# Kernel optimization log

Hardware: AMD Instinct MI355X
Metric: run time of the kernel (lower is better)

Reference implementation:

```python
import jax, jax.numpy as jnp
import numpy as np
from jax import lax

D_MODEL = 192
D_STATE = 128
D_CONV = 3
EXPAND = 2
HEADDIM = 64
NGROUPS = 1
CHUNK = 256
K = 4  # scan directions
D_INNER = EXPAND * D_MODEL          # 384
D_SSM = D_INNER                     # 384
NHEADS = D_SSM // HEADDIM           # 6
HH = K * NHEADS                     # 24 heads total (dir-major)
CONV_CH = D_SSM + 2 * NGROUPS * D_STATE + NHEADS  # 646 (conv applied to x,B,C,dt channels)
D_IN_PROJ = 2 * D_INNER + 2 * NGROUPS * D_STATE + NHEADS  # 1030
BSZ, HIMG, WIMG = 4, 64, 64


def setup_inputs() -> dict:
    key = jax.random.key(0)
    ks = jax.random.split(key, 8)
    u = jax.random.normal(ks[0], (BSZ, HIMG, WIMG, D_MODEL), jnp.float32)
    W_in = jax.random.normal(ks[1], (D_MODEL, D_IN_PROJ), jnp.float32) * 0.02
    conv_w = jax.random.normal(ks[2], (CONV_CH, 1, D_CONV, D_CONV), jnp.float32) * 0.1
    conv_b = jnp.zeros((CONV_CH,), jnp.float32)
    # dt_bias init per source: inverse-softplus of dt ~ LogUniform(1e-3, 1e-1), tiled over 4 dirs
    dt = jnp.exp(jax.random.uniform(ks[3], (NHEADS,)) * (np.log(0.1) - np.log(0.001)) + np.log(0.001))
    dt = jnp.maximum(dt, 1e-4)
    inv_dt = dt + jnp.log(-jnp.expm1(-dt))
    dt_bias = jnp.tile(inv_dt[None, :], (K, 1))  # (4, nheads)
    A = jax.random.uniform(ks[4], (NHEADS,), minval=1.0, maxval=16.0)
    A_logs = jnp.tile(jnp.log(A), (K,))          # (24,)
    Ds = jnp.ones((HH,), jnp.float32)
    norm_w = jnp.ones((D_SSM,), jnp.float32)
    W_out = jax.random.normal(ks[5], (D_INNER, D_MODEL), jnp.float32) * 0.02
    return dict(u=u, W_in=W_in, conv_w=conv_w, conv_b=conv_b, dt_bias=dt_bias,
                A_logs=A_logs, Ds=Ds, norm_w=norm_w, W_out=W_out)


def _ssd(x, dt, A, Bm, Cm, chunk):
    """Chunked selective state-space scan (Mamba2 SSD).
    x: (b,L,H,P), dt: (b,L,H) (post-softplus), A: (H,) negative scalars,
    Bm/Cm: (b,L,G,N) with heads grouped G-major (H = G*hpg)."""
    b, L, H, P = x.shape
    G, N = Bm.shape[2], Bm.shape[3]
    hpg = H // G
    nc = L // chunk
    x = x.reshape(b, nc, chunk, G, hpg, P)
    dt = dt.reshape(b, nc, chunk, G, hpg)
    Bm = Bm.reshape(b, nc, chunk, G, N)
    Cm = Cm.reshape(b, nc, chunk, G, N)
    dA = dt * A.reshape(G, hpg)                 # (b,z,c,g,h), negative
    dAc = jnp.cumsum(dA, axis=2)                # within-chunk cumsum
    dAt = jnp.transpose(dAc, (0, 1, 3, 4, 2))   # (b,z,g,h,c)
    idx = jnp.arange(chunk)
    mask = idx[:, None] >= idx[None, :]         # causal within chunk
    seg = jnp.exp(jnp.where(mask, dAt[..., :, None] - dAt[..., None, :], -1e30))  # (b,z,g,h,c,s)
    CB = jnp.einsum('bzcgn,bzsgn->bzgcs', Cm, Bm)
    xdt = x * dt[..., None]                     # dt applied at source position
    y_intra = jnp.einsum('bzghcs,bzsghp->bzcghp', CB[:, :, :, None] * seg, xdt)
    decay_last = jnp.exp(dAc[:, :, -1:] - dAc)  # (b,z,c,g,h)
    states = jnp.einsum('bzcgn,bzcghp->bzghpn', Bm, xdt * decay_last[..., None])
    cd = jnp.exp(dAc[:, :, -1])                 # (b,z,g,h) whole-chunk decay

    def step(carry, inp):
        s, c = inp
        return carry * c[..., None, None] + s, carry  # emit state entering the chunk

    _, prevs = lax.scan(step, jnp.zeros_like(states[:, 0]),
                        (jnp.swapaxes(states, 0, 1), jnp.swapaxes(cd, 0, 1)))
    prev = jnp.swapaxes(prevs, 0, 1)            # (b,z,g,h,P,N)
    y_inter = jnp.einsum('bzcgn,bzghpn->bzcghp', Cm, prev) * jnp.exp(dAc)[..., None]
    return (y_intra + y_inter).reshape(b, L, H, P)


def reference(u, W_in, conv_w, conv_b, dt_bias, A_logs, Ds, norm_w, W_out):
    B, H, W, C = u.shape
    L = H * W
    zxbcdt = u @ W_in                            # (B,H,W,1030); d_mlp == 0
    z = zxbcdt[..., :D_SSM]                      # gate
    xBCdt = zxbcdt[..., D_SSM:]                  # (B,H,W,CONV_CH)
    # depthwise 3x3 conv + SiLU (NCHW)
    xb = jnp.transpose(xBCdt, (0, 3, 1, 2))
    xb = lax.conv_general_dilated(xb, conv_w, (1, 1), 'SAME',
                                  feature_group_count=CONV_CH,
                                  dimension_numbers=('NCHW', 'OIHW', 'NCHW'))
    xb = jax.nn.silu(xb + conv_b[None, :, None, None])
    # 4 scan directions: row-major, col-major, and their reverses
    d0 = xb.reshape(B, CONV_CH, L)
    d1 = jnp.transpose(xb, (0, 1, 3, 2)).reshape(B, CONV_CH, L)
    dirs = jnp.stack([d0, d1], axis=1)
    dirs = jnp.concatenate([dirs, jnp.flip(dirs, axis=-1)], axis=1)  # (B,4,CONV_CH,L)
    seq = jnp.transpose(dirs, (0, 3, 1, 2))      # (B,L,4,CONV_CH)
    xs = seq[..., :D_SSM].reshape(B, L, HH, HEADDIM)
    Bs = seq[..., D_SSM:D_SSM + D_STATE]         # (B,L,4,N), ngroups=1 -> G=4 dirs
    Cs = seq[..., D_SSM + D_STATE:D_SSM + 2 * D_STATE]
    dts = seq[..., D_SSM + 2 * D_STATE:].reshape(B, L, HH)
    dt = jax.nn.softplus(dts + dt_bias.reshape(HH))
    A = -jnp.exp(A_logs)                         # (HH,)
    y = _ssd(xs, dt, A, Bs, Cs, CHUNK) + xs * Ds[None, None, :, None]
    y = y.reshape(B, L, K, D_SSM)
    y0 = y[:, :, 0]
    y1 = y[:, :, 1]
    y2 = jnp.flip(y[:, :, 2], axis=1)
    y3 = jnp.flip(y[:, :, 3], axis=1)
    wh1 = jnp.transpose(y1.reshape(B, W, H, D_SSM), (0, 2, 1, 3)).reshape(B, L, D_SSM)
    wh3 = jnp.transpose(y3.reshape(B, W, H, D_SSM), (0, 2, 1, 3)).reshape(B, L, D_SSM)
    out = (y0 + y2 + wh1 + wh3).reshape(B, H, W, D_SSM)
    # RMSNormGated (norm_before_gate=False, group_size = d_ssm)
    g = out * jax.nn.silu(z)
    g = g * lax.rsqrt(jnp.mean(g * g, axis=-1, keepdims=True) + 1e-5) * norm_w
    return g @ W_out
```

## Files before the change

### kernel.cpp

```cpp
#include <hip/hip_runtime.h>
#include <hip/hip_fp16.h>
#include <math.h>

#define BQ 4
#define LQ 4096
#define DM 192
#define DIP 1030
#define DSSM 384
#define DST 128
#define CCH 646
#define CH640 640
#define NHD 6
#define KDIR 4
#define NCH 16
#define CLEN 256
#define UH_ELEMS (16384 * 192)
#define WT_ELEMS (1152 * 192)
#define WO_ELEMS (192 * 384)

using half8 = __attribute__((ext_vector_type(8))) _Float16;
using half4 = __attribute__((ext_vector_type(4))) _Float16;
using f32x4 = __attribute__((ext_vector_type(4))) float;

#define XWI(pp, ss) ((pp) * 72 + ((((ss) >> 3) ^ ((pp) >> 3)) << 3) + ((ss) & 7))
#define XW2(n, ss) ((n) * 72 + (((((ss) >> 3) ^ ((n) >> 3)) & 7) << 3) + ((ss) & 7))

__device__ __forceinline__ int pixof(int k, int t) {
  switch (k) {
    case 0: return t;
    case 1: return ((t & 63) << 6) | (t >> 6);
    case 2: return 4095 - t;
    default: { int tp = 4095 - t; return ((tp & 63) << 6) | (tp >> 6); }
  }
}

__device__ __forceinline__ float softplusf(float x) {
  return (x > 20.f) ? x : log1pf(expf(x));
}
__device__ __forceinline__ float siluf(float x) {
  return x / (1.f + __expf(-x));
}

__global__ void k_cvt(const float* __restrict__ u, const float* __restrict__ W,
                      const float* __restrict__ Wout,
                      _Float16* __restrict__ uh, _Float16* __restrict__ whT,
                      _Float16* __restrict__ woT) {
  int idx = blockIdx.x * 256 + threadIdx.x;
  if (idx < UH_ELEMS) uh[idx] = (_Float16)u[idx];
  int widx = idx - UH_ELEMS;
  if (widx >= 0 && widx < WT_ELEMS) {
    int n = widx / 192, kk = widx - n * 192;
    whT[widx] = (n < DIP) ? (_Float16)W[(size_t)kk * DIP + n] : (_Float16)0.f;
  }
  int wo = idx - UH_ELEMS - WT_ELEMS;
  if (wo >= 0 && wo < WO_ELEMS) {
    int n = wo / 384, kk = wo - n * 384;
    woT[wo] = (_Float16)Wout[(size_t)kk * DM + n];
  }
}

__global__ __launch_bounds__(256) void k_inproj(
    const _Float16* __restrict__ uh, const _Float16* __restrict__ whT,
    __half* __restrict__ zh, __half* __restrict__ xbch, float* __restrict__ xdt32) {
  __shared__ __align__(16) _Float16 sA[128 * 72];
  __shared__ __align__(16) _Float16 sB[128 * 72];
  int nt = blockIdx.x, mt = blockIdx.y;
  int m0 = mt * 128, n0 = nt * 128;
  int t = threadIdx.x, lane = t & 63, w = t >> 6;
  int acol = lane & 15, koff = (lane >> 4) * 8;
  int wr = w >> 1, wc = w & 1;
  f32x4 zz = {0.f, 0.f, 0.f, 0.f};
  f32x4 acc[4][4];
#pragma unroll
  for (int fr = 0; fr < 4; ++fr)
#pragma unroll
    for (int fc = 0; fc < 4; ++fc) acc[fr][fc] = zz;
  for (int kk = 0; kk < 3; ++kk) {
    if (kk) __syncthreads();
#pragma unroll
    for (int i = 0; i < 4; ++i) {
      int task = t + i * 256;
      int row = task >> 3, oct = task & 7;
      *(half8*)&sA[row * 72 + oct * 8] =
          *(const half8*)&uh[(size_t)(m0 + row) * 192 + kk * 64 + oct * 8];
      *(half8*)&sB[row * 72 + oct * 8] =
          *(const half8*)&whT[(size_t)(n0 + row) * 192 + kk * 64 + oct * 8];
    }
    __syncthreads();
#pragma unroll
    for (int ks = 0; ks < 2; ++ks) {
      half8 af[4], bf[4];
#pragma unroll
      for (int f = 0; f < 4; ++f) {
        af[f] = *(const half8*)&sA[(wr * 64 + f * 16 + acol) * 72 + ks * 32 + koff];
        bf[f] = *(const half8*)&sB[(wc * 64 + f * 16 + acol) * 72 + ks * 32 + koff];
      }
#pragma unroll
      for (int fr = 0; fr < 4; ++fr)
#pragma unroll
        for (int fc = 0; fc < 4; ++fc)
          acc[fr][fc] = __builtin_amdgcn_mfma_f32_16x16x32_f16(af[fr], bf[fc], acc[fr][fc], 0, 0, 0);
    }
  }
  int rb = (lane >> 4) * 4;
#pragma unroll
  for (int fr = 0; fr < 4; ++fr) {
#pragma unroll
    for (int fc = 0; fc < 4; ++fc) {
      int n = n0 + wc * 64 + fc * 16 + acol;
#pragma unroll
      for (int r = 0; r < 4; ++r) {
        int m = m0 + wr * 64 + fr * 16 + rb + r;
        float v = acc[fr][fc][r];
        if (n < DSSM) zh[(size_t)m * DSSM + n] = (__half)v;
        else if (n < 1024) xbch[(size_t)m * CH640 + (n - DSSM)] = (__half)v;
        else if (n < DIP) xdt32[(size_t)m * NHD + (n - 1024)] = v;
      }
    }
  }
}

__global__ void k_conv(const __half* __restrict__ xbch, const float* __restrict__ xdt,
                       const float* __restrict__ cw, const float* __restrict__ cb,
                       __half* __restrict__ convh, float* __restrict__ dtraw) {
  int pid = blockIdx.x;
  int b = pid >> 12, p = pid & 4095;
  int y = p >> 6, x = p & 63;
  int t = threadIdx.x;
  const __half2* baseh2 = (const __half2*)(xbch + (size_t)b * LQ * CH640);
  __half2* outh2 = (__half2*)(convh + (size_t)pid * CH640);
  for (int pc = t; pc < 320; pc += 256) {
    int c0 = pc * 2;
    float s0 = 0.f, s1 = 0.f;
#pragma unroll
    for (int ky = 0; ky < 3; ++ky) {
      int yy = y + ky - 1;
      if (yy < 0 || yy > 63) continue;
#pragma unroll
      for (int kx = 0; kx < 3; ++kx) {
        int xx = x + kx - 1;
        if (xx < 0 || xx > 63) continue;
        __half2 v = baseh2[(size_t)(yy * 64 + xx) * 320 + pc];
        int wi = ky * 3 + kx;
        s0 += (float)v.x * cw[c0 * 9 + wi];
        s1 += (float)v.y * cw[(c0 + 1) * 9 + wi];
      }
    }
    __half2 o;
    o.x = (__half)siluf(s0 + cb[c0]);
    o.y = (__half)siluf(s1 + cb[c0 + 1]);
    outh2[pc] = o;
  }
  if (t < NHD) {
    const float* based = xdt + (size_t)b * LQ * NHD;
    float s = 0.f;
#pragma unroll
    for (int ky = 0; ky < 3; ++ky) {
      int yy = y + ky - 1;
      if (yy < 0 || yy > 63) continue;
#pragma unroll
      for (int kx = 0; kx < 3; ++kx) {
        int xx = x + kx - 1;
        if (xx < 0 || xx > 63) continue;
        s += based[(size_t)(yy * 64 + xx) * NHD + t] * cw[(CH640 + t) * 9 + ky * 3 + kx];
      }
    }
    dtraw[(size_t)pid * NHD + t] = siluf(s + cb[CH640 + t]);
  }
}

__global__ void k_prep(const float* __restrict__ dtraw, const float* __restrict__ dt_bias,
                       const float* __restrict__ A_logs,
                       float* __restrict__ dtb, float* __restrict__ dacb) {
  __shared__ float sb[CLEN];
  int z = blockIdx.x, k = blockIdx.y, b = blockIdx.z;
  int s = threadIdx.x;
  int pixel = pixof(k, z * CLEN + s);
  const float* row = dtraw + ((size_t)(b * LQ + pixel)) * NHD;
  float raw[NHD];
#pragma unroll
  for (int h = 0; h < NHD; ++h) raw[h] = row[h];
  size_t base = (((size_t)(b * KDIR + k) * NCH + z) * NHD) * CLEN;
  for (int h = 0; h < NHD; ++h) {
    float dtv = softplusf(raw[h] + dt_bias[k * NHD + h]);
    float dA = dtv * (-expf(A_logs[k * NHD + h]));
    sb[s] = dA;
    __syncthreads();
    for (int off = 1; off < CLEN; off <<= 1) {
      float v = (s >= off) ? sb[s - off] : 0.f;
      __syncthreads();
      sb[s] += v;
      __syncthreads();
    }
    dtb[base + (size_t)h * CLEN + s] = dtv;
    dacb[base + (size_t)h * CLEN + s] = sb[s];
    __syncthreads();
  }
}

__global__ __launch_bounds__(256, 4) void k_cb(const _Float16* __restrict__ convh,
                                               _Float16* __restrict__ cbuf) {
  __shared__ __align__(16) char smem[34816];
  _Float16* sCt = (_Float16*)smem;
  _Float16* sBt = (_Float16*)(smem + 17408);
  int pi = blockIdx.x, z = blockIdx.y, bk = blockIdx.z;
  int b = bk >> 2, kd = bk & 3;
  int SI = 0;
  while ((SI + 1) * (SI + 2) / 2 <= pi) ++SI;
  int SJ = pi - SI * (SI + 1) / 2;
  int t = threadIdx.x, lane = t & 63, w = t >> 6;
  int acol = lane & 15, koff = (lane >> 4) * 8;
  int R = w * 16, arow = R + acol, rbase = R + (lane >> 4) * 4;
  const _Float16* convb = convh + (size_t)b * LQ * CH640;
  for (int i = 0; i < 4; ++i) {
    int c = t + i * 256;
    int row = c >> 4, seg = c & 15;
    int pc = pixof(kd, z * CLEN + SI * 64 + row);
    *(half8*)&sCt[row * 136 + seg * 8] =
        *(const half8*)&convb[(size_t)pc * CH640 + (DSSM + DST) + seg * 8];
    int pbx = pixof(kd, z * CLEN + SJ * 64 + row);
    *(half8*)&sBt[row * 136 + seg * 8] =
        *(const half8*)&convb[(size_t)pbx * CH640 + DSSM + seg * 8];
  }
  __syncthreads();
  f32x4 zz = {0.f, 0.f, 0.f, 0.f};
  f32x4 acc[4] = {zz, zz, zz, zz};
  for (int ks = 0; ks < 4; ++ks) {
    half8 a = *(const half8*)&sCt[arow * 136 + ks * 32 + koff];
#pragma unroll
    for (int cg = 0; cg < 4; ++cg) {
      half8 bf = *(const half8*)&sBt[(cg * 16 + acol) * 136 + ks * 32 + koff];
      acc[cg] = __builtin_amdgcn_mfma_f32_16x16x32_f16(a, bf, acc[cg], 0, 0, 0);
    }
  }
  size_t base = ((size_t)(bk * NCH + z) * 10 + pi) * 4096;
#pragma unroll
  for (int cg = 0; cg < 4; ++cg)
#pragma unroll
    for (int r = 0; r < 4; ++r)
      cbuf[base + (size_t)(rbase + r) * 64 + cg * 16 + acol] = (_Float16)acc[cg][r];
}

__global__ void k_diag(const _Float16* __restrict__ cbuf, const float* __restrict__ dacb,
                       _Float16* __restrict__ dbuf) {
  __shared__ float sd[64];
  int hs = blockIdx.x;
  int si = hs / 6, h = hs % 6;
  int z = blockIdx.y, bk = blockIdx.z;
  int t = threadIdx.x;
  if (t < 64) sd[t] = dacb[(((size_t)bk * NCH + z) * NHD + h) * CLEN + si * 64 + t];
  __syncthreads();
  size_t cb = ((size_t)(bk * NCH + z) * 10 + si * (si + 1) / 2 + si) * 4096;
  size_t db = (((size_t)(bk * NCH + z) * 4 + si) * NHD + h) * 4096;
#pragma unroll
  for (int i = 0; i < 16; ++i) {
    int e = t + i * 256;
    int sl = e >> 6, ss = e & 63;
    _Float16 v = (_Float16)0.f;
    if (ss <= sl) v = (_Float16)((float)cbuf[cb + e] * __expf(sd[sl] - sd[ss]));
    dbuf[db + e] = v;
  }
}

__global__ __launch_bounds__(256, 4) void k_states(
    const _Float16* __restrict__ convh, const float* __restrict__ dtb,
    const float* __restrict__ dacb, _Float16* __restrict__ statesT) {
  __shared__ __align__(16) _Float16 sA[64 * 72];
  __shared__ __align__(16) _Float16 sB2[128 * 72];
  __shared__ float sFac[CLEN];
  int h = blockIdx.x, z = blockIdx.y, bk = blockIdx.z;
  int b = bk >> 2, kd = bk & 3;
  int t = threadIdx.x, lane = t & 63, w = t >> 6;
  int acol = lane & 15, koct = lane >> 4;
  size_t dbase = (((size_t)bk * NCH + z) * NHD + h) * CLEN;
  {
    float dac_last = dacb[dbase + CLEN - 1];
    sFac[t] = dtb[dbase + t] * __expf(dac_last - dacb[dbase + t]);
  }
  __syncthreads();
  const _Float16* convb = convh + (size_t)b * LQ * CH640;
  f32x4 zz = {0.f, 0.f, 0.f, 0.f};
  f32x4 acc[8] = {zz, zz, zz, zz, zz, zz, zz, zz};
  for (int st = 0; st < 4; ++st) {
    if (st) __syncthreads();
#pragma unroll
    for (int i = 0; i < 2; ++i) {
      int c = t + i * 256;
      int ss = c >> 3, pp0 = (c & 7) * 8;
      int sg = st * 64 + ss;
      int px = pixof(kd, z * CLEN + sg);
      half8 xv = *(const half8*)&convb[(size_t)px * CH640 + h * 64 + pp0];
      float f = sFac[sg];
#pragma unroll
      for (int u = 0; u < 8; ++u) sA[XWI(pp0 + u, ss)] = (_Float16)((float)xv[u] * f);
    }
#pragma unroll
    for (int i = 0; i < 4; ++i) {
      int c = t + i * 256;
      int ss = c >> 4, n0 = (c & 15) * 8;
      int sg = st * 64 + ss;
      int px = pixof(kd, z * CLEN + sg);
      half8 bv = *(const half8*)&convb[(size_t)px * CH640 + DSSM + n0];
#pragma unroll
      for (int u = 0; u < 8; ++u) sB2[XW2(n0 + u, ss)] = bv[u];
    }
    __syncthreads();
#pragma unroll
    for (int ks = 0; ks < 2; ++ks) {
      int kso = ks * 4 + koct;
      int arow = w * 16 + acol;
      half8 a = *(const half8*)&sA[arow * 72 + ((kso ^ (arow >> 3)) << 3)];
#pragma unroll
      for (int nf = 0; nf < 8; ++nf) {
        int col = nf * 16 + acol;
        half8 bf = *(const half8*)&sB2[col * 72 + (((kso ^ (col >> 3)) & 7) << 3)];
        acc[nf] = __builtin_amdgcn_mfma_f32_16x16x32_f16(a, bf, acc[nf], 0, 0, 0);
      }
    }
  }
  size_t sbase = (((size_t)bk * NCH + z) * NHD + h) * (128 * 64);
  int rbase = koct * 4;
#pragma unroll
  for (int nf = 0; nf < 8; ++nf) {
    int col = nf * 16 + acol;
#pragma unroll
    for (int r = 0; r < 4; ++r)
      statesT[sbase + (size_t)(w * 16 + rbase + r) * 128 + col] = (_Float16)acc[nf][r];
  }
}

__global__ void k_scan(_Float16* __restrict__ states, const float* __restrict__ dacb) {
  int h = blockIdx.x, k = blockIdx.y, b = blockIdx.z;
  int bk = b * KDIR + k;
  int t = threadIdx.x;
  float carry[32];
#pragma unroll
  for (int j = 0; j < 32; ++j) carry[j] = 0.f;
  for (int z = 0; z < NCH; ++z) {
    float cd = __expf(dacb[(((size_t)bk * NCH + z) * NHD + h) * CLEN + (CLEN - 1)]);
    size_t sbase = (((size_t)bk * NCH + z) * NHD + h) * (128 * 64);
#pragma unroll
    for (int j = 0; j < 32; ++j) {
      size_t idx = sbase + (size_t)j * 256 + t;
      float sv = (float)states[idx];
      states[idx] = (_Float16)carry[j];
      carry[j] = carry[j] * cd + sv;
    }
  }
}

__global__ __launch_bounds__(256, 8) void k_y(
    const _Float16* __restrict__ convh, const float* __restrict__ dtb,
    const float* __restrict__ dacb, const _Float16* __restrict__ cbuf,
    const _Float16* __restrict__ prevT, const _Float16* __restrict__ dbuf,
    const float* __restrict__ Ds, _Float16* __restrict__ ybuf) {
  __shared__ __align__(16) _Float16 sXW[64 * 72];
  __shared__ float sdt[CLEN], sdac[CLEN], sFac[CLEN];
  __shared__ float sExpD[64], sRs[64];

  int wg = blockIdx.x;
  int xid = (wg & 7) * 768 + (wg >> 3);
  int grp = xid / 24, i24 = xid % 24;
  int h = i24 >> 2, si_t = i24 & 3;
  int bk = grp >> 4, z = grp & 15;
  int b = bk >> 2, kd = bk & 3;
  int t = threadIdx.x, lane = t & 63, w = t >> 6;
  int acol = lane & 15, koff = (lane >> 4) * 8;
  int R = w * 16, arow = R + acol, rbase = R + (lane >> 4) * 4;

  size_t dbase = (((size_t)bk * NCH + z) * NHD + h) * CLEN;
  sdt[t] = dtb[dbase + t];
  sdac[t] = dacb[dbase + t];
  __syncthreads();
  float ref = sdac[si_t * 64];
  sFac[t] = __expf(ref - sdac[t]);
  if (t < 64) {
    float d = sdac[si_t * 64 + t];
    sExpD[t] = __expf(d);
    sRs[t] = __expf(d - ref);
  }
  const _Float16* convb = convh + (size_t)b * LQ * CH640;
  const _Float16* pbp = prevT + (((size_t)bk * NCH + z) * NHD + h) * (128 * 64);
  f32x4 zz = {0.f, 0.f, 0.f, 0.f};
  f32x4 accE[4] = {zz, zz, zz, zz};
  f32x4 accI[4] = {zz, zz, zz, zz};
  int pxa = pixof(kd, z * CLEN + si_t * 64 + arow);
#pragma unroll
  for (int ks = 0; ks < 4; ++ks) {
    half8 a = *(const half8*)&convb[(size_t)pxa * CH640 + (DSSM + DST) + ks * 32 + koff];
#pragma unroll
    for (int cg = 0; cg < 4; ++cg) {
      half8 bf = *(const half8*)&pbp[(size_t)(cg * 16 + acol) * 128 + ks * 32 + koff];
      accE[cg] = __builtin_amdgcn_mfma_f32_16x16x32_f16(a, bf, accE[cg], 0, 0, 0);
    }
  }
  __syncthreads();
  for (int SJ = 0; SJ < si_t; ++SJ) {
#pragma unroll
    for (int i = 0; i < 2; ++i) {
      int c = t + i * 256;
      int ss = c >> 3, pp0 = (c & 7) * 8;
      int sg = SJ * 64 + ss;
      int px = pixof(kd, z * CLEN + sg);
      half8 xv = *(const half8*)&convb[(size_t)px * CH640 + h * 64 + pp0];
      float f = sdt[sg] * sFac[sg];
#pragma unroll
      for (int u = 0; u < 8; ++u)
        sXW[XWI(pp0 + u, ss)] = (_Float16)((float)xv[u] * f);
    }
    __syncthreads();
    size_t cbase = ((size_t)(bk * NCH + z) * 10 + si_t * (si_t + 1) / 2 + SJ) * 4096;
#pragma unroll
    for (int ks = 0; ks < 2; ++ks) {
      half8 a = *(const half8*)&cbuf[cbase + (size_t)arow * 64 + ks * 32 + koff];
      int kso = ks * 4 + (lane >> 4);
#pragma unroll
      for (int cg = 0; cg < 4; ++cg) {
        int col = cg * 16 + acol;
        half8 bf = *(const half8*)&sXW[col * 72 + ((kso ^ (col >> 3)) << 3)];
        accI[cg] = __builtin_amdgcn_mfma_f32_16x16x32_f16(a, bf, accI[cg], 0, 0, 0);
      }
    }
    __syncthreads();
  }
  {
    float rsv[4];
#pragma unroll
    for (int r = 0; r < 4; ++r) rsv[r] = sRs[rbase + r];
#pragma unroll
    for (int cg = 0; cg < 4; ++cg)
#pragma unroll
      for (int r = 0; r < 4; ++r) accI[cg][r] *= rsv[r];
  }
  {
#pragma unroll
    for (int i = 0; i < 2; ++i) {
      int c = t + i * 256;
      int ss = c >> 3, pp0 = (c & 7) * 8;
      int sg = si_t * 64 + ss;
      int px = pixof(kd, z * CLEN + sg);
      half8 xv = *(const half8*)&convb[(size_t)px * CH640 + h * 64 + pp0];
      float f = sdt[sg];
#pragma unroll
      for (int u = 0; u < 8; ++u)
        sXW[XWI(pp0 + u, ss)] = (_Float16)((float)xv[u] * f);
    }
    __syncthreads();
    size_t db = (((size_t)(bk * NCH + z) * 4 + si_t) * NHD + h) * 4096;
#pragma unroll
    for (int ks = 0; ks < 2; ++ks) {
      half8 a = *(const half8*)&dbuf[db + (size_t)arow * 64 + ks * 32 + koff];
      int kso = ks * 4 + (lane >> 4);
#pragma unroll
      for (int cg = 0; cg < 4; ++cg) {
        int col = cg * 16 + acol;
        half8 bf = *(const half8*)&sXW[col * 72 + ((kso ^ (col >> 3)) << 3)];
        accI[cg] = __builtin_amdgcn_mfma_f32_16x16x32_f16(a, bf, accI[cg], 0, 0, 0);
      }
    }
  }
  float dsv = Ds[kd * NHD + h];
  float eD[4];
#pragma unroll
  for (int r = 0; r < 4; ++r) eD[r] = sExpD[rbase + r];
#pragma unroll
  for (int cg = 0; cg < 4; ++cg) {
    int col = cg * 16 + acol;
#pragma unroll
    for (int r = 0; r < 4; ++r) {
      int row = rbase + r;
      int tg = z * CLEN + si_t * 64 + row;
      int px = pixof(kd, tg);
      float xv = (float)convb[(size_t)px * CH640 + h * 64 + col];
      float yv = accI[cg][r] + eD[r] * accE[cg][r] + dsv * xv;
      ybuf[((size_t)bk * LQ + tg) * DSSM + h * 64 + col] = (_Float16)yv;
    }
  }
}

__global__ __launch_bounds__(256) void k_final(
    const _Float16* __restrict__ yb, const _Float16* __restrict__ zh,
    const float* __restrict__ norm_w, const _Float16* __restrict__ woT,
    float* __restrict__ out) {
  __shared__ __align__(16) _Float16 sG[32 * 392];
  int m0 = blockIdx.x * 32;
  int t = threadIdx.x;
  int row = t >> 3, q = t & 7;
  int m = m0 + row, b = m >> 12, px = m & 4095;
  int tr = ((px & 63) << 6) | (px >> 6);
  int t0 = px, t1 = tr, t2 = 4095 - px, t3 = 4095 - tr;
  size_t b4 = (size_t)b * 4;
  float gbuf[48];
  float sumsq = 0.f;
#pragma unroll
  for (int i = 0; i < 6; ++i) {
    int c0 = q * 48 + i * 8;
    half8 y0 = *(const half8*)&yb[((b4 + 0) * LQ + t0) * DSSM + c0];
    half8 y1 = *(const half8*)&yb[((b4 + 1) * LQ + t1) * DSSM + c0];
    half8 y2 = *(const half8*)&yb[((b4 + 2) * LQ + t2) * DSSM + c0];
    half8 y3 = *(const half8*)&yb[((b4 + 3) * LQ + t3) * DSSM + c0];
    half8 zv8 = *(const half8*)&zh[(size_t)m * DSSM + c0];
#pragma unroll
    for (int u = 0; u < 8; ++u) {
      float zv = (float)zv8[u];
      float g = ((float)y0[u] + (float)y1[u] + (float)y2[u] + (float)y3[u]) *
                (zv / (1.f + __expf(-zv)));
      gbuf[i * 8 + u] = g;
      sumsq += g * g;
    }
  }
  sumsq += __shfl_xor(sumsq, 1);
  sumsq += __shfl_xor(sumsq, 2);
  sumsq += __shfl_xor(sumsq, 4);
  float rstd = rsqrtf(sumsq / (float)DSSM + 1e-5f);
#pragma unroll
  for (int i = 0; i < 6; ++i) {
    int c0 = q * 48 + i * 8;
    half8 gv;
#pragma unroll
    for (int u = 0; u < 8; ++u)
      gv[u] = (_Float16)(gbuf[i * 8 + u] * rstd * norm_w[c0 + u]);
    *(half8*)&sG[row * 392 + c0] = gv;
  }
  __syncthreads();
  int lane = t & 63, w = t >> 6;
  int acol = lane & 15, koff = (lane >> 4) * 8;
  int rt = (w & 1) * 16, cb0 = (w >> 1) * 96;
  f32x4 zz = {0.f, 0.f, 0.f, 0.f};
  f32x4 acc[6] = {zz, zz, zz, zz, zz, zz};
  for (int ks = 0; ks < 12; ++ks) {
    half8 a = *(const half8*)&sG[(rt + acol) * 392 + ks * 32 + koff];
#pragma unroll
    for (int nf = 0; nf < 6; ++nf) {
      half8 bf = *(const half8*)&woT[(size_t)(cb0 + nf * 16 + acol) * 384 + ks * 32 + koff];
      acc[nf] = __builtin_amdgcn_mfma_f32_16x16x32_f16(a, bf, acc[nf], 0, 0, 0);
    }
  }
  int rb = (lane >> 4) * 4;
#pragma unroll
  for (int nf = 0; nf < 6; ++nf) {
    int n = cb0 + nf * 16 + acol;
#pragma unroll
    for (int r = 0; r < 4; ++r)
      out[(size_t)(m0 + rt + rb + r) * DM + n] = acc[nf][r];
  }
}

extern "C" void kernel_launch(void* const* d_in, const int* in_sizes, int n_in,
                              void* d_out, int out_size, void* d_ws, size_t ws_size,
                              hipStream_t stream) {
  const float* u = (const float*)d_in[0];
  const float* W_in = (const float*)d_in[1];
  const float* conv_w = (const float*)d_in[2];
  const float* conv_b = (const float*)d_in[3];
  const float* dt_bias = (const float*)d_in[4];
  const float* A_logs = (const float*)d_in[5];
  const float* Ds = (const float*)d_in[6];
  const float* norm_w = (const float*)d_in[7];
  const float* W_out = (const float*)d_in[8];
  float* out = (float*)d_out;

  float* ws = (float*)d_ws;
  size_t off = 0;
  __half* zh = (__half*)(ws + off); off += (size_t)BQ * LQ * DSSM / 2;
  float* scratch = ws + off; off += 1683456;
  _Float16* uh = (_Float16*)scratch;
  _Float16* whT = uh + UH_ELEMS;
  float* dtraw = scratch;
  float* dtb = scratch + 98304;
  float* dacb = scratch + 98304 + 393216;
  __half* xbch = (__half*)(ws + off); off += (size_t)BQ * LQ * CH640 / 2;
  float* xdt32 = ws + off; off += (size_t)BQ * LQ * NHD;
  __half* convh = (__half*)(ws + off); off += (size_t)BQ * LQ * CH640 / 2;
  _Float16* statesT = (_Float16*)(ws + off); off += (size_t)BQ * KDIR * NCH * NHD * 128 * 64 / 2;
  __half* ybuf = (__half*)(ws + off); off += (size_t)BQ * KDIR * LQ * DSSM / 2;
  _Float16* dbuf = (_Float16*)(ws + off); off += (size_t)BQ * KDIR * NCH * 4 * NHD * 4096 / 2;
  _Float16* woT = (_Float16*)(ws + off); off += WO_ELEMS / 2;
  _Float16* cbuf = (_Float16*)xbch;

  k_cvt<<<(UH_ELEMS + WT_ELEMS + WO_ELEMS + 255) / 256, 256, 0, stream>>>(u, W_in, W_out, uh, whT, woT);
  k_inproj<<<dim3(9, 128), 256, 0, stream>>>(uh, whT, zh, xbch, xdt32);
  k_conv<<<BQ * LQ, 256, 0, stream>>>(xbch, xdt32, conv_w, conv_b, convh, dtraw);
  k_prep<<<dim3(NCH, KDIR, BQ), 256, 0, stream>>>(dtraw, dt_bias, A_logs, dtb, dacb);
  k_cb<<<dim3(10, NCH, BQ * KDIR), 256, 0, stream>>>((const _Float16*)convh, cbuf);
  k_diag<<<dim3(24, NCH, BQ * KDIR), 256, 0, stream>>>(cbuf, dacb, dbuf);
  k_states<<<dim3(NHD, NCH, BQ * KDIR), 256, 0, stream>>>((const _Float16*)convh, dtb, dacb, statesT);
  k_scan<<<dim3(NHD, KDIR, BQ), 256, 0, stream>>>(statesT, dacb);
  k_y<<<KDIR * NHD * 4 * NCH * BQ, 256, 0, stream>>>((const _Float16*)convh, dtb, dacb,
                                                     (const _Float16*)cbuf, statesT, dbuf, Ds,
                                                     (_Float16*)ybuf);
  k_final<<<BQ * LQ / 32, 256, 0, stream>>>((const _Float16*)ybuf, (const _Float16*)zh,
                                            norm_w, woT, out);
}
```

Measured before the change: 445.9 us.

## Precompute decay-scaled X tiles once in new kernel, reuse across k_y off-diagonal blocks

A new k_xw kernel computes each 64-row sub-tile of dt*exp(dac_end - dac)*x once and stores it transposed in a global buffer. k_y then reads these tiles directly for its off-diagonal intra-chunk products and fixes up the decay with a per-subtile scalar applied to the C·B fragment, instead of rebuilding the scaled tile in shared memory on every loop iteration. This drops most of the syncthreads and shared-memory staging in k_y. The cost is an extra launch, an extra workspace buffer with its write and read traffic, fp16 rescaling of the C·B fragment that may lose precision, and a lower occupancy hint on k_y.

```diff
diff --git a/kernel.cpp b/kernel.cpp
--- a/kernel.cpp
+++ b/kernel.cpp
@@ -262,6 +262,40 @@
   }
 }
 
+__global__ void k_xw(const _Float16* __restrict__ convh, const float* __restrict__ dtb,
+                     const float* __restrict__ dacb, _Float16* __restrict__ xwnT) {
+  __shared__ __align__(16) _Float16 sA[64 * 72];
+  int th = blockIdx.x;
+  int tile = th / 6, h = th % 6;
+  int z = blockIdx.y, bk = blockIdx.z;
+  int b = bk >> 2, kd = bk & 3;
+  int t = threadIdx.x;
+  size_t dbase = (((size_t)bk * NCH + z) * NHD + h) * CLEN;
+  float dacE = dacb[dbase + tile * 64 + 63];
+  const _Float16* convb = convh + (size_t)b * LQ * CH640;
+#pragma unroll
+  for (int i = 0; i < 2; ++i) {
+    int c = t + i * 256;
+    int ss = c >> 3, pp0 = (c & 7) * 8;
+    int sg = tile * 64 + ss;
+    int px = pixof(kd, z * CLEN + sg);
+    half8 xv = *(const half8*)&convb[(size_t)px * CH640 + h * 64 + pp0];
+    float f = dtb[dbase + sg] * __expf(dacE - dacb[dbase + sg]);
+#pragma unroll
+    for (int u = 0; u < 8; ++u) sA[XWI(pp0 + u, ss)] = (_Float16)((float)xv[u] * f);
+  }
+  __syncthreads();
+  size_t obase = (((size_t)(bk * NCH + z) * 4 + tile) * NHD + h) * 4096;
+#pragma unroll
+  for (int i = 0; i < 2; ++i) {
+    int task = t + i * 256;
+    int p = task >> 3, q = task & 7;
+    half8 v = *(const half8*)&sA[p * 72 + (q << 3)];
+    int ss0 = (q ^ (p >> 3)) << 3;
+    *(half8*)&xwnT[obase + p * 64 + ss0] = v;
+  }
+}
+
 __global__ __launch_bounds__(256, 4) void k_states(
     const _Float16* __restrict__ convh, const float* __restrict__ dtb,
     const float* __restrict__ dacb, _Float16* __restrict__ statesT) {
@@ -349,14 +383,13 @@
   }
 }
 
-__global__ __launch_bounds__(256, 8) void k_y(
+__global__ __launch_bounds__(256, 4) void k_y(
     const _Float16* __restrict__ convh, const float* __restrict__ dtb,
     const float* __restrict__ dacb, const _Float16* __restrict__ cbuf,
     const _Float16* __restrict__ prevT, const _Float16* __restrict__ dbuf,
-    const float* __restrict__ Ds, _Float16* __restrict__ ybuf) {
+    const _Float16* __restrict__ xwnT, const float* __restrict__ Ds,
+    _Float16* __restrict__ ybuf) {
   __shared__ __align__(16) _Float16 sXW[64 * 72];
-  __shared__ float sdt[CLEN], sdac[CLEN], sFac[CLEN];
-  __shared__ float sExpD[64], sRs[64];
 
   int wg = blockIdx.x;
   int xid = (wg & 7) * 768 + (wg >> 3);
@@ -369,21 +402,37 @@
   int R = w * 16, arow = R + acol, rbase = R + (lane >> 4) * 4;
 
   size_t dbase = (((size_t)bk * NCH + z) * NHD + h) * CLEN;
-  sdt[t] = dtb[dbase + t];
-  sdac[t] = dacb[dbase + t];
-  __syncthreads();
-  float ref = sdac[si_t * 64];
-  sFac[t] = __expf(ref - sdac[t]);
-  if (t < 64) {
-    float d = sdac[si_t * 64 + t];
-    sExpD[t] = __expf(d);
-    sRs[t] = __expf(d - ref);
-  }
   const _Float16* convb = convh + (size_t)b * LQ * CH640;
-  const _Float16* pbp = prevT + (((size_t)bk * NCH + z) * NHD + h) * (128 * 64);
+
+#pragma unroll
+  for (int i = 0; i < 2; ++i) {
+    int c = t + i * 256;
+    int ss = c >> 3, pp0 = (c & 7) * 8;
+    int sg = si_t * 64 + ss;
+    int px = pixof(kd, z * CLEN + sg);
+    half8 xv = *(const half8*)&convb[(size_t)px * CH640 + h * 64 + pp0];
+    float f = dtb[dbase + sg];
+#pragma unroll
+    for (int u = 0; u < 8; ++u)
+      sXW[XWI(pp0 + u, ss)] = (_Float16)((float)xv[u] * f);
+  }
+
+  float ref = dacb[dbase + si_t * 64];
+  float4 dv = *(const float4*)&dacb[dbase + si_t * 64 + rbase];
+  float eD[4], rsv[4];
+  {
+    float dvv[4] = {dv.x, dv.y, dv.z, dv.w};
+#pragma unroll
+    for (int r = 0; r < 4; ++r) {
+      eD[r] = __expf(dvv[r]);
+      rsv[r] = __expf(dvv[r] - ref);
+    }
+  }
+
   f32x4 zz = {0.f, 0.f, 0.f, 0.f};
   f32x4 accE[4] = {zz, zz, zz, zz};
   f32x4 accI[4] = {zz, zz, zz, zz};
+  const _Float16* pbp = prevT + (((size_t)bk * NCH + z) * NHD + h) * (128 * 64);
   int pxa = pixof(kd, z * CLEN + si_t * 64 + arow);
 #pragma unroll
   for (int ks = 0; ks < 4; ++ks) {
@@ -394,25 +443,33 @@
       accE[cg] = __builtin_amdgcn_mfma_f32_16x16x32_f16(a, bf, accE[cg], 0, 0, 0);
     }
   }
-  __syncthreads();
   for (int SJ = 0; SJ < si_t; ++SJ) {
-#pragma unroll
-    for (int i = 0; i < 2; ++i) {
-      int c = t + i * 256;
-      int ss = c >> 3, pp0 = (c & 7) * 8;
-      int sg = SJ * 64 + ss;
-      int px = pixof(kd, z * CLEN + sg);
-      half8 xv = *(const half8*)&convb[(size_t)px * CH640 + h * 64 + pp0];
-      float f = sdt[sg] * sFac[sg];
-#pragma unroll
-      for (int u = 0; u < 8; ++u)
-        sXW[XWI(pp0 + u, ss)] = (_Float16)((float)xv[u] * f);
-    }
-    __syncthreads();
+    _Float16 suh = (_Float16)__expf(ref - dacb[dbase + SJ * 64 + 63]);
     size_t cbase = ((size_t)(bk * NCH + z) * 10 + si_t * (si_t + 1) / 2 + SJ) * 4096;
+    const _Float16* xwb = xwnT + (((size_t)(bk * NCH + z) * 4 + SJ) * NHD + h) * 4096;
 #pragma unroll
     for (int ks = 0; ks < 2; ++ks) {
       half8 a = *(const half8*)&cbuf[cbase + (size_t)arow * 64 + ks * 32 + koff];
+#pragma unroll
+      for (int u = 0; u < 8; ++u) a[u] = a[u] * suh;
+#pragma unroll
+      for (int cg = 0; cg < 4; ++cg) {
+        int col = cg * 16 + acol;
+        half8 bf = *(const half8*)&xwb[(size_t)col * 64 + ks * 32 + koff];
+        accI[cg] = __builtin_amdgcn_mfma_f32_16x16x32_f16(a, bf, accI[cg], 0, 0, 0);
+      }
+    }
+  }
+#pragma unroll
+  for (int cg = 0; cg < 4; ++cg)
+#pragma unroll
+    for (int r = 0; r < 4; ++r) accI[cg][r] *= rsv[r];
+  __syncthreads();
+  {
+    size_t db = (((size_t)(bk * NCH + z) * 4 + si_t) * NHD + h) * 4096;
+#pragma unroll
+    for (int ks = 0; ks < 2; ++ks) {
+      half8 a = *(const half8*)&dbuf[db + (size_t)arow * 64 + ks * 32 + koff];
       int kso = ks * 4 + (lane >> 4);
 #pragma unroll
       for (int cg = 0; cg < 4; ++cg) {
@@ -421,48 +478,8 @@
         accI[cg] = __builtin_amdgcn_mfma_f32_16x16x32_f16(a, bf, accI[cg], 0, 0, 0);
       }
     }
-    __syncthreads();
-  }
-  {
-    float rsv[4];
-#pragma unroll
-    for (int r = 0; r < 4; ++r) rsv[r] = sRs[rbase + r];
-#pragma unroll
-    for (int cg = 0; cg < 4; ++cg)
-#pragma unroll
-      for (int r = 0; r < 4; ++r) accI[cg][r] *= rsv[r];
-  }
-  {
-#pragma unroll
-    for (int i = 0; i < 2; ++i) {
-      int c = t + i * 256;
-      int ss = c >> 3, pp0 = (c & 7) * 8;
-      int sg = si_t * 64 + ss;
-      int px = pixof(kd, z * CLEN + sg);
-      half8 xv = *(const half8*)&convb[(size_t)px * CH640 + h * 64 + pp0];
-      float f = sdt[sg];
-#pragma unroll
-      for (int u = 0; u < 8; ++u)
-        sXW[XWI(pp0 + u, ss)] = (_Float16)((float)xv[u] * f);
-    }
-    __syncthreads();
-    size_t db = (((size_t)(bk * NCH + z) * 4 + si_t) * NHD + h) * 4096;
-#pragma unroll
-    for (int ks = 0; ks < 2; ++ks) {
-      half8 a = *(const half8*)&dbuf[db + (size_t)arow * 64 + ks * 32 + koff];
-      int kso = ks * 4 + (lane >> 4);
-#pragma unroll
-      for (int cg = 0; cg < 4; ++cg) {
-        int col = cg * 16 + acol;
-        half8 bf = *(const half8*)&sXW[col * 72 + ((kso ^ (col >> 3)) << 3)];
-        accI[cg] = __builtin_amdgcn_mfma_f32_16x16x32_f16(a, bf, accI[cg], 0, 0, 0);
-      }
-    }
   }
   float dsv = Ds[kd * NHD + h];
-  float eD[4];
-#pragma unroll
-  for (int r = 0; r < 4; ++r) eD[r] = sExpD[rbase + r];
 #pragma unroll
   for (int cg = 0; cg < 4; ++cg) {
     int col = cg * 16 + acol;
@@ -576,6 +593,7 @@
   __half* ybuf = (__half*)(ws + off); off += (size_t)BQ * KDIR * LQ * DSSM / 2;
   _Float16* dbuf = (_Float16*)(ws + off); off += (size_t)BQ * KDIR * NCH * 4 * NHD * 4096 / 2;
   _Float16* woT = (_Float16*)(ws + off); off += WO_ELEMS / 2;
+  _Float16* xwnT = (_Float16*)(ws + off); off += (size_t)BQ * KDIR * NCH * 4 * NHD * 4096 / 2;
   _Float16* cbuf = (_Float16*)xbch;
 
   k_cvt<<<(UH_ELEMS + WT_ELEMS + WO_ELEMS + 255) / 256, 256, 0, stream>>>(u, W_in, W_out, uh, whT, woT);
@@ -584,11 +602,12 @@
   k_prep<<<dim3(NCH, KDIR, BQ), 256, 0, stream>>>(dtraw, dt_bias, A_logs, dtb, dacb);
   k_cb<<<dim3(10, NCH, BQ * KDIR), 256, 0, stream>>>((const _Float16*)convh, cbuf);
   k_diag<<<dim3(24, NCH, BQ * KDIR), 256, 0, stream>>>(cbuf, dacb, dbuf);
+  k_xw<<<dim3(24, NCH, BQ * KDIR), 256, 0, stream>>>((const _Float16*)convh, dtb, dacb, xwnT);
   k_states<<<dim3(NHD, NCH, BQ * KDIR), 256, 0, stream>>>((const _Float16*)convh, dtb, dacb, statesT);
   k_scan<<<dim3(NHD, KDIR, BQ), 256, 0, stream>>>(statesT, dacb);
   k_y<<<KDIR * NHD * 4 * NCH * BQ, 256, 0, stream>>>((const _Float16*)convh, dtb, dacb,
-                                                     (const _Float16*)cbuf, statesT, dbuf, Ds,
-                                                     (_Float16*)ybuf);
+                                                     (const _Float16*)cbuf, statesT, dbuf,
+                                                     xwnT, Ds, (_Float16*)ybuf);
   k_final<<<BQ * LQ / 32, 256, 0, stream>>>((const _Float16*)ybuf, (const _Float16*)zh,
                                             norm_w, woT, out);
 }
```

Result: slower. 501.0 us (+12.4%).
